# Kernel optimization log

Measured on AMD Instinct MI355X. Metric: run time of the kernel, lower is better.

The kernel has to match this reference:

```python
import jax, jax.numpy as jnp
import numpy as np

INPUT_SIZE = 128
HIDDEN_SIZE = 256
OUTPUT_SIZE = 64
BATCH = 128
SEQ_LEN = 2048


def _xavier(key, shape):
    fan_in, fan_out = shape[1], shape[0]
    std = (2.0 / (fan_in + fan_out)) ** 0.5
    return jax.random.normal(key, shape, dtype=jnp.float32) * std


def setup_inputs() -> dict:
    key = jax.random.key(0)
    ks = jax.random.split(key, 5)
    gru_in = INPUT_SIZE + OUTPUT_SIZE  # Jordan feedback: input concat prev output
    return {
        "x": jax.random.normal(ks[0], (BATCH, SEQ_LEN, INPUT_SIZE), dtype=jnp.float32),
        "w_ih": _xavier(ks[1], (3 * HIDDEN_SIZE, gru_in)),   # [r|z|n] input weights
        "w_hh": _xavier(ks[2], (3 * HIDDEN_SIZE, HIDDEN_SIZE)),
        "b_ih": jnp.zeros((3 * HIDDEN_SIZE,), dtype=jnp.float32),
        "b_hh": jnp.zeros((3 * HIDDEN_SIZE,), dtype=jnp.float32),
        "fc_w": _xavier(ks[3], (OUTPUT_SIZE, HIDDEN_SIZE)),
        "fc_b": jnp.zeros((OUTPUT_SIZE,), dtype=jnp.float32),
    }


def reference(x, w_ih, w_hh, b_ih, b_hh, fc_w, fc_b):
    B = x.shape[0]
    H = w_hh.shape[1]
    O = fc_w.shape[0]

    def step(carry, x_t):
        h, y_prev = carry  # h: [B,H], y_prev: [B,O]
        inp = jnp.concatenate([x_t, y_prev], axis=-1)       # [B, I+O]
        gi = inp @ w_ih.T + b_ih                            # [B, 3H]
        gh = h @ w_hh.T + b_hh                              # [B, 3H]
        i_r, i_z, i_n = jnp.split(gi, 3, axis=-1)
        h_r, h_z, h_n = jnp.split(gh, 3, axis=-1)
        r = jax.nn.sigmoid(i_r + h_r)
        z = jax.nn.sigmoid(i_z + h_z)
        n = jnp.tanh(i_n + r * h_n)
        h_new = (1.0 - z) * n + z * h                       # PyTorch GRU update
        y = jnp.tanh(h_new @ fc_w.T + fc_b)                 # Jordan output feedback
        return (h_new, y), None

    xs = jnp.swapaxes(x, 0, 1)  # [T, B, I] for scan over time
    h0 = jnp.zeros((B, H), dtype=x.dtype)
    y0 = jnp.zeros((B, O), dtype=x.dtype)
    (h_last, y_last), _ = jax.lax.scan(step, (h0, y0), xs)
    return y_last  # matches outputs[:, -1, :]
```

## Files before the change

### kernel.cpp

```cpp
#include <hip/hip_runtime.h>
#include <math.h>


#define TSTEPS 2048
#define ISZ 128

typedef _Float16 half8 __attribute__((ext_vector_type(8)));
typedef float f32x4 __attribute__((ext_vector_type(4)));
typedef unsigned int u32;
typedef unsigned int u32x4 __attribute__((ext_vector_type(4)));
typedef unsigned long long u64;

__device__ __forceinline__ f32x4 mfma16(half8 a, half8 b, f32x4 c) {
  return __builtin_amdgcn_mfma_f32_16x16x32_f16(a, b, c, 0, 0, 0);
}
__device__ __forceinline__ float sigm(float x) {
  return __builtin_amdgcn_rcpf(1.f + __expf(-x));
}
__device__ __forceinline__ float tanh_fast(float x) {
  return 1.f - 2.f * __builtin_amdgcn_rcpf(1.f + __expf(2.f * x));
}

__device__ __forceinline__ void st_pkt(void* p, u32x4 v) {
  asm volatile("global_store_dwordx4 %0, %1, off sc1" :: "v"(p), "v"(v) : "memory");
}
__device__ __forceinline__ void ld_pkt3_issue(const void* p1, const void* p2,
                                              const void* p3, u32x4& r1, u32x4& r2,
                                              u32x4& r3) {
  asm volatile("global_load_dwordx4 %0, %3, off sc1\n\t"
               "global_load_dwordx4 %1, %4, off sc1\n\t"
               "global_load_dwordx4 %2, %5, off sc1"
               : "=&v"(r1), "=&v"(r2), "=&v"(r3)
               : "v"(p1), "v"(p2), "v"(p3) : "memory");
}
__device__ __forceinline__ void ld_pkt3_wait(const void* p1, const void* p2,
                                             const void* p3, u32x4& r1, u32x4& r2,
                                             u32x4& r3) {
  asm volatile("global_load_dwordx4 %0, %3, off sc1\n\t"
               "global_load_dwordx4 %1, %4, off sc1\n\t"
               "global_load_dwordx4 %2, %5, off sc1\n\t"
               "s_waitcnt vmcnt(0)"
               : "=&v"(r1), "=&v"(r2), "=&v"(r3)
               : "v"(p1), "v"(p2), "v"(p3) : "memory");
}

__global__ __attribute__((amdgpu_flat_work_group_size(256, 256),
                          amdgpu_waves_per_eu(1, 1)))
void jordan_rnn(const float* __restrict__ xg, const float* __restrict__ w_ih,
                const float* __restrict__ w_hh, const float* __restrict__ b_ih,
                const float* __restrict__ b_hh, const float* __restrict__ fc_w,
                const float* __restrict__ fc_b, float* __restrict__ out,
                unsigned char* __restrict__ ws)
{
  const int tid  = threadIdx.x;
  const int lane = tid & 63;
  const int wv   = tid >> 6;
  const int n    = lane & 15;
  const int quad = lane >> 4;
  const int col  = blockIdx.x & 7;
  const int q    = blockIdx.x >> 3;
  const int u0   = q * 64 + wv * 16;
  const int b0   = col * 16;

  unsigned char* pay = ws;

  __shared__ _Float16 act[16][456];
  {
    unsigned int* za = (unsigned int*)&act[0][0];
    for (int i = tid; i < 3648; i += 256) za[i] = 0u;
  }

  half8 wr[14], wz[14], win[6], whn[8], wfc[8];
  {
    const int kq = quad * 8;
    const int ur = u0 + n, uz = 256 + u0 + n, un = 512 + u0 + n;
#pragma unroll
    for (int kk = 0; kk < 6; ++kk) {
      const float* pr = w_ih + ur * 192 + kk * 32 + kq;
      const float* pz = w_ih + uz * 192 + kk * 32 + kq;
      const float* pn = w_ih + un * 192 + kk * 32 + kq;
#pragma unroll
      for (int j = 0; j < 8; ++j) {
        wr[kk][j] = (_Float16)pr[j]; wz[kk][j] = (_Float16)pz[j]; win[kk][j] = (_Float16)pn[j];
      }
    }
#pragma unroll
    for (int kk = 0; kk < 8; ++kk) {
      const float* pr = w_hh + ur * 256 + kk * 32 + kq;
      const float* pz = w_hh + uz * 256 + kk * 32 + kq;
      const float* pn = w_hh + un * 256 + kk * 32 + kq;
#pragma unroll
      for (int j = 0; j < 8; ++j) {
        wr[6 + kk][j] = (_Float16)pr[j]; wz[6 + kk][j] = (_Float16)pz[j]; whn[kk][j] = (_Float16)pn[j];
      }
    }
#pragma unroll
    for (int kk = 0; kk < 8; ++kk) {
      const float* pf = fc_w + (wv * 16 + n) * 256 + kk * 32 + kq;
#pragma unroll
      for (int j = 0; j < 8; ++j) wfc[kk][j] = (_Float16)pf[j];
    }
  }
  const float br   = b_ih[u0 + n] + b_hh[u0 + n];
  const float bz   = b_ih[256 + u0 + n] + b_hh[256 + u0 + n];
  const float bin_ = b_ih[512 + u0 + n];
  const float bhn  = b_hh[512 + u0 + n];
  const float fcb  = fc_b[wv * 16 + n];

  float hprev[4] = {0.f, 0.f, 0.f, 0.f};

  const int xr = tid >> 4, xc = tid & 15;
  const int prow = lane >> 2, pc4 = lane & 3;
  const int sblk = tid >> 6, srem = tid & 63;
  const int srow = srem >> 2, sc4 = srem & 3;
  const int ok0 = 6 + 2 * q;
  const int fk0 = 2 * q;
  const int q1 = (q + 1) & 3, q2 = (q + 2) & 3, q3 = (q + 3) & 3;

  unsigned char* cb0 = pay + (size_t)col * 16384;
  unsigned char* cb1 = cb0 + 131072;
  const int poff = (q * 4 + wv) * 1024 + lane * 16;
  const int off1 = (q1 * 4 + sblk) * 1024 + srem * 16;
  const int off2 = (q2 * 4 + sblk) * 1024 + srem * 16;
  const int off3 = (q3 * 4 + sblk) * 1024 + srem * 16;

  const float* xbase = xg + (size_t)(b0 + xr) * TSTEPS * ISZ + xc * 8;
  float4 xv0, xv1;

  {
    float4 a = *(const float4*)xbase, b = *(const float4*)(xbase + 4);
    union { _Float16 h[8]; uint4 u; } pk;
    pk.h[0]=(_Float16)a.x; pk.h[1]=(_Float16)a.y; pk.h[2]=(_Float16)a.z; pk.h[3]=(_Float16)a.w;
    pk.h[4]=(_Float16)b.x; pk.h[5]=(_Float16)b.y; pk.h[6]=(_Float16)b.z; pk.h[7]=(_Float16)b.w;
    *(uint4*)&act[xr][xc * 8] = pk.u;
    xv0 = *(const float4*)(xbase + ISZ);
    xv1 = *(const float4*)(xbase + ISZ + 4);
  }
  __syncthreads();

  for (int t = 1; t <= TSTEPS; ++t) {
    const u32 tgt = (u32)(t - 1);
    unsigned char* cb = ((t - 1) & 1) ? cb1 : cb0;

    u32x4 r1, r2, r3;
    ld_pkt3_issue(cb + off1, cb + off2, cb + off3, r1, r2, r3);

    {
      u64 v = *(const u64*)&act[prow][192 + u0 + pc4 * 4];
      u32x4 pkt;
      pkt[0] = (u32)v; pkt[1] = (u32)(v >> 32); pkt[2] = tgt; pkt[3] = 0u;
      st_pkt(cb + poff, pkt);
    }

    f32x4 aR = {0,0,0,0}, aZ = {0,0,0,0}, aIN = {0,0,0,0}, aHN = {0,0,0,0};
    f32x4 accy = {0,0,0,0};
#pragma unroll
    for (int kk = 0; kk < 4; ++kk) {
      half8 af = *(const half8*)&act[n][kk * 32 + quad * 8];
      aR = mfma16(af, wr[kk], aR);
      aZ = mfma16(af, wz[kk], aZ);
      aIN = mfma16(af, win[kk], aIN);
    }
#pragma unroll
    for (int kk = 0; kk < 2; ++kk) {
      half8 af = *(const half8*)&act[n][(ok0 + kk) * 32 + quad * 8];
      aR = mfma16(af, wr[ok0 + kk], aR);
      aZ = mfma16(af, wz[ok0 + kk], aZ);
      aHN = mfma16(af, whn[ok0 - 6 + kk], aHN);
    }
#pragma unroll
    for (int kk = 0; kk < 2; ++kk) {
      half8 af = *(const half8*)&act[n][192 + (fk0 + kk) * 32 + quad * 8];
      accy = mfma16(af, wfc[fk0 + kk], accy);
    }

    __builtin_amdgcn_sched_barrier(0);
    asm volatile("s_waitcnt vmcnt(1)" : "+v"(r1), "+v"(r2), "+v"(r3) :: "memory");
    __builtin_amdgcn_sched_barrier(0);
    {
      int ok = (r1[2] >= tgt) && (r2[2] >= tgt) && (r3[2] >= tgt);
      while (!__all(ok)) {
        ld_pkt3_wait(cb + off1, cb + off2, cb + off3, r1, r2, r3);
        ok = (r1[2] >= tgt) && (r2[2] >= tgt) && (r3[2] >= tgt);
      }
    }
    *(u64*)&act[srow][192 + q1 * 64 + sblk * 16 + sc4 * 4] = ((u64)r1[1] << 32) | r1[0];
    *(u64*)&act[srow][192 + q2 * 64 + sblk * 16 + sc4 * 4] = ((u64)r2[1] << 32) | r2[0];
    *(u64*)&act[srow][192 + q3 * 64 + sblk * 16 + sc4 * 4] = ((u64)r3[1] << 32) | r3[0];
    __syncthreads();

#pragma unroll
    for (int kk = 6; kk < 14; ++kk) {
      if (kk == ok0 || kk == ok0 + 1) continue;
      half8 af = *(const half8*)&act[n][kk * 32 + quad * 8];
      aR = mfma16(af, wr[kk], aR);
      aZ = mfma16(af, wz[kk], aZ);
      aHN = mfma16(af, whn[kk - 6], aHN);
    }
#pragma unroll
    for (int kk = 0; kk < 8; ++kk) {
      if (kk == fk0 || kk == fk0 + 1) continue;
      half8 af = *(const half8*)&act[n][192 + kk * 32 + quad * 8];
      accy = mfma16(af, wfc[kk], accy);
    }
    if (t > 1) {
#pragma unroll
      for (int r = 0; r < 4; ++r)
        act[quad * 4 + r][128 + wv * 16 + n] = (_Float16)tanh_fast(accy[r] + fcb);
    }
    {
      union { _Float16 h[8]; uint4 u; } pk;
      pk.h[0]=(_Float16)xv0.x; pk.h[1]=(_Float16)xv0.y; pk.h[2]=(_Float16)xv0.z; pk.h[3]=(_Float16)xv0.w;
      pk.h[4]=(_Float16)xv1.x; pk.h[5]=(_Float16)xv1.y; pk.h[6]=(_Float16)xv1.z; pk.h[7]=(_Float16)xv1.w;
      *(uint4*)&act[xr][xc * 8] = pk.u;
      const size_t ts = (t + 1 < TSTEPS) ? (size_t)(t + 1) : (size_t)(TSTEPS - 1);
      xv0 = *(const float4*)(xbase + ts * ISZ);
      xv1 = *(const float4*)(xbase + ts * ISZ + 4);
    }
    __syncthreads();

#pragma unroll
    for (int kk = 4; kk < 6; ++kk) {
      half8 af = *(const half8*)&act[n][kk * 32 + quad * 8];
      aR = mfma16(af, wr[kk], aR);
      aZ = mfma16(af, wz[kk], aZ);
      aIN = mfma16(af, win[kk], aIN);
    }
#pragma unroll
    for (int r = 0; r < 4; ++r) {
      float rg = sigm(aR[r] + br);
      float zg = sigm(aZ[r] + bz);
      float nn = tanh_fast(aIN[r] + bin_ + rg * (aHN[r] + bhn));
      float hv = (1.f - zg) * nn + zg * hprev[r];
      hprev[r] = hv;
      act[quad * 4 + r][192 + u0 + n] = (_Float16)hv;
    }
    __syncthreads();
  }

  {
    const u32 tgt = (u32)TSTEPS;
    unsigned char* cb = (TSTEPS & 1) ? cb1 : cb0;

    u32x4 r1, r2, r3;
    ld_pkt3_issue(cb + off1, cb + off2, cb + off3, r1, r2, r3);
    {
      u64 v = *(const u64*)&act[prow][192 + u0 + pc4 * 4];
      u32x4 pkt;
      pkt[0] = (u32)v; pkt[1] = (u32)(v >> 32); pkt[2] = tgt; pkt[3] = 0u;
      st_pkt(cb + poff, pkt);
    }

    f32x4 accy = {0,0,0,0};
#pragma unroll
    for (int kk = 0; kk < 2; ++kk) {
      half8 af = *(const half8*)&act[n][192 + (fk0 + kk) * 32 + quad * 8];
      accy = mfma16(af, wfc[fk0 + kk], accy);
    }

    __builtin_amdgcn_sched_barrier(0);
    asm volatile("s_waitcnt vmcnt(1)" : "+v"(r1), "+v"(r2), "+v"(r3) :: "memory");
    __builtin_amdgcn_sched_barrier(0);
    {
      int ok = (r1[2] >= tgt) && (r2[2] >= tgt) && (r3[2] >= tgt);
      while (!__all(ok)) {
        ld_pkt3_wait(cb + off1, cb + off2, cb + off3, r1, r2, r3);
        ok = (r1[2] >= tgt) && (r2[2] >= tgt) && (r3[2] >= tgt);
      }
    }
    *(u64*)&act[srow][192 + q1 * 64 + sblk * 16 + sc4 * 4] = ((u64)r1[1] << 32) | r1[0];
    *(u64*)&act[srow][192 + q2 * 64 + sblk * 16 + sc4 * 4] = ((u64)r2[1] << 32) | r2[0];
    *(u64*)&act[srow][192 + q3 * 64 + sblk * 16 + sc4 * 4] = ((u64)r3[1] << 32) | r3[0];
    __syncthreads();

#pragma unroll
    for (int kk = 0; kk < 8; ++kk) {
      if (kk == fk0 || kk == fk0 + 1) continue;
      half8 af = *(const half8*)&act[n][192 + kk * 32 + quad * 8];
      accy = mfma16(af, wfc[kk], accy);
    }
    if (q == 0) {
#pragma unroll
      for (int r = 0; r < 4; ++r)
        out[(size_t)(b0 + quad * 4 + r) * 64 + wv * 16 + n] = tanh_fast(accy[r] + fcb);
    }
  }
}

extern "C" void kernel_launch(void* const* d_in, const int* in_sizes, int n_in,
                              void* d_out, int out_size, void* d_ws, size_t ws_size,
                              hipStream_t stream) {
  hipMemsetAsync(d_ws, 0, 262144, stream);
  jordan_rnn<<<dim3(32), dim3(256), 0, stream>>>(
      (const float*)d_in[0], (const float*)d_in[1], (const float*)d_in[2],
      (const float*)d_in[3], (const float*)d_in[4], (const float*)d_in[5],
      (const float*)d_in[6], (float*)d_out, (unsigned char*)d_ws);
}
```

Baseline: 4.573 ms.

## Publish hidden-state packets right after gate compute with checksum validation

Each block now sends its new hidden slice to peer blocks straight from registers at the end of the step, in MFMA column layout, rather than re-reading it from LDS at the start of the next step. This puts the send earlier on the cross-block critical path. An XOR checksum field guards against torn 16-byte packets, the poll loop gains an s_sleep, and only the q==0 blocks run the final exchange. In exchange, receivers now do scalar half-word LDS stores, wait for all loads instead of all but one, and may pick up extra latency from the sleep.

```diff
diff --git a/kernel.cpp b/kernel.cpp
--- a/kernel.cpp
+++ b/kernel.cpp
@@ -43,6 +43,7 @@
                : "=&v"(r1), "=&v"(r2), "=&v"(r3)
                : "v"(p1), "v"(p2), "v"(p3) : "memory");
 }
+#define PKT_OK(r, tgt) (((r)[2] >= (tgt)) && (((r)[0] ^ (r)[1] ^ (r)[2]) == (r)[3]))
 
 __global__ __attribute__((amdgpu_flat_work_group_size(256, 256),
                           amdgpu_waves_per_eu(1, 1)))
@@ -110,9 +111,9 @@
   float hprev[4] = {0.f, 0.f, 0.f, 0.f};
 
   const int xr = tid >> 4, xc = tid & 15;
-  const int prow = lane >> 2, pc4 = lane & 3;
   const int sblk = tid >> 6, srem = tid & 63;
-  const int srow = srem >> 2, sc4 = srem & 3;
+  const int cr = (srem >> 4) * 4;
+  const int cc = srem & 15;
   const int ok0 = 6 + 2 * q;
   const int fk0 = 2 * q;
   const int q1 = (q + 1) & 3, q2 = (q + 2) & 3, q3 = (q + 3) & 3;
@@ -145,13 +146,6 @@
     u32x4 r1, r2, r3;
     ld_pkt3_issue(cb + off1, cb + off2, cb + off3, r1, r2, r3);
 
-    {
-      u64 v = *(const u64*)&act[prow][192 + u0 + pc4 * 4];
-      u32x4 pkt;
-      pkt[0] = (u32)v; pkt[1] = (u32)(v >> 32); pkt[2] = tgt; pkt[3] = 0u;
-      st_pkt(cb + poff, pkt);
-    }
-
     f32x4 aR = {0,0,0,0}, aZ = {0,0,0,0}, aIN = {0,0,0,0}, aHN = {0,0,0,0};
     f32x4 accy = {0,0,0,0};
 #pragma unroll
@@ -175,18 +169,28 @@
     }
 
     __builtin_amdgcn_sched_barrier(0);
-    asm volatile("s_waitcnt vmcnt(1)" : "+v"(r1), "+v"(r2), "+v"(r3) :: "memory");
+    asm volatile("s_waitcnt vmcnt(0)" : "+v"(r1), "+v"(r2), "+v"(r3) :: "memory");
     __builtin_amdgcn_sched_barrier(0);
     {
-      int ok = (r1[2] >= tgt) && (r2[2] >= tgt) && (r3[2] >= tgt);
+      int ok = PKT_OK(r1, tgt) && PKT_OK(r2, tgt) && PKT_OK(r3, tgt);
       while (!__all(ok)) {
+        __builtin_amdgcn_s_sleep(1);
         ld_pkt3_wait(cb + off1, cb + off2, cb + off3, r1, r2, r3);
-        ok = (r1[2] >= tgt) && (r2[2] >= tgt) && (r3[2] >= tgt);
-      }
-    }
-    *(u64*)&act[srow][192 + q1 * 64 + sblk * 16 + sc4 * 4] = ((u64)r1[1] << 32) | r1[0];
-    *(u64*)&act[srow][192 + q2 * 64 + sblk * 16 + sc4 * 4] = ((u64)r2[1] << 32) | r2[0];
-    *(u64*)&act[srow][192 + q3 * 64 + sblk * 16 + sc4 * 4] = ((u64)r3[1] << 32) | r3[0];
+        ok = PKT_OK(r1, tgt) && PKT_OK(r2, tgt) && PKT_OK(r3, tgt);
+      }
+    }
+    {
+      union { u64 u; _Float16 h[4]; } w1, w2, w3;
+      w1.u = ((u64)r1[1] << 32) | r1[0];
+      w2.u = ((u64)r2[1] << 32) | r2[0];
+      w3.u = ((u64)r3[1] << 32) | r3[0];
+#pragma unroll
+      for (int r = 0; r < 4; ++r) {
+        act[cr + r][192 + q1 * 64 + sblk * 16 + cc] = w1.h[r];
+        act[cr + r][192 + q2 * 64 + sblk * 16 + cc] = w2.h[r];
+        act[cr + r][192 + q3 * 64 + sblk * 16 + cc] = w3.h[r];
+      }
+    }
     __syncthreads();
 
 #pragma unroll
@@ -226,30 +230,35 @@
       aZ = mfma16(af, wz[kk], aZ);
       aIN = mfma16(af, win[kk], aIN);
     }
-#pragma unroll
-    for (int r = 0; r < 4; ++r) {
-      float rg = sigm(aR[r] + br);
-      float zg = sigm(aZ[r] + bz);
-      float nn = tanh_fast(aIN[r] + bin_ + rg * (aHN[r] + bhn));
-      float hv = (1.f - zg) * nn + zg * hprev[r];
-      hprev[r] = hv;
-      act[quad * 4 + r][192 + u0 + n] = (_Float16)hv;
+    {
+      union { _Float16 h[4]; u64 u; } ph;
+#pragma unroll
+      for (int r = 0; r < 4; ++r) {
+        float rg = sigm(aR[r] + br);
+        float zg = sigm(aZ[r] + bz);
+        float nn = tanh_fast(aIN[r] + bin_ + rg * (aHN[r] + bhn));
+        float hv = (1.f - zg) * nn + zg * hprev[r];
+        hprev[r] = hv;
+        ph.h[r] = (_Float16)hv;
+      }
+      unsigned char* cbw = (t & 1) ? cb1 : cb0;
+      u32x4 pkt;
+      pkt[0] = (u32)ph.u; pkt[1] = (u32)(ph.u >> 32); pkt[2] = (u32)t;
+      pkt[3] = pkt[0] ^ pkt[1] ^ pkt[2];
+      st_pkt(cbw + poff, pkt);
+#pragma unroll
+      for (int r = 0; r < 4; ++r)
+        act[quad * 4 + r][192 + u0 + n] = ph.h[r];
     }
     __syncthreads();
   }
 
-  {
+  if (q == 0) {
     const u32 tgt = (u32)TSTEPS;
     unsigned char* cb = (TSTEPS & 1) ? cb1 : cb0;
 
     u32x4 r1, r2, r3;
     ld_pkt3_issue(cb + off1, cb + off2, cb + off3, r1, r2, r3);
-    {
-      u64 v = *(const u64*)&act[prow][192 + u0 + pc4 * 4];
-      u32x4 pkt;
-      pkt[0] = (u32)v; pkt[1] = (u32)(v >> 32); pkt[2] = tgt; pkt[3] = 0u;
-      st_pkt(cb + poff, pkt);
-    }
 
     f32x4 accy = {0,0,0,0};
 #pragma unroll
@@ -259,18 +268,28 @@
     }
 
     __builtin_amdgcn_sched_barrier(0);
-    asm volatile("s_waitcnt vmcnt(1)" : "+v"(r1), "+v"(r2), "+v"(r3) :: "memory");
+    asm volatile("s_waitcnt vmcnt(0)" : "+v"(r1), "+v"(r2), "+v"(r3) :: "memory");
     __builtin_amdgcn_sched_barrier(0);
     {
-      int ok = (r1[2] >= tgt) && (r2[2] >= tgt) && (r3[2] >= tgt);
+      int ok = PKT_OK(r1, tgt) && PKT_OK(r2, tgt) && PKT_OK(r3, tgt);
       while (!__all(ok)) {
+        __builtin_amdgcn_s_sleep(1);
         ld_pkt3_wait(cb + off1, cb + off2, cb + off3, r1, r2, r3);
-        ok = (r1[2] >= tgt) && (r2[2] >= tgt) && (r3[2] >= tgt);
-      }
-    }
-    *(u64*)&act[srow][192 + q1 * 64 + sblk * 16 + sc4 * 4] = ((u64)r1[1] << 32) | r1[0];
-    *(u64*)&act[srow][192 + q2 * 64 + sblk * 16 + sc4 * 4] = ((u64)r2[1] << 32) | r2[0];
-    *(u64*)&act[srow][192 + q3 * 64 + sblk * 16 + sc4 * 4] = ((u64)r3[1] << 32) | r3[0];
+        ok = PKT_OK(r1, tgt) && PKT_OK(r2, tgt) && PKT_OK(r3, tgt);
+      }
+    }
+    {
+      union { u64 u; _Float16 h[4]; } w1, w2, w3;
+      w1.u = ((u64)r1[1] << 32) | r1[0];
+      w2.u = ((u64)r2[1] << 32) | r2[0];
+      w3.u = ((u64)r3[1] << 32) | r3[0];
+#pragma unroll
+      for (int r = 0; r < 4; ++r) {
+        act[cr + r][192 + q1 * 64 + sblk * 16 + cc] = w1.h[r];
+        act[cr + r][192 + q2 * 64 + sblk * 16 + cc] = w2.h[r];
+        act[cr + r][192 + q3 * 64 + sblk * 16 + cc] = w3.h[r];
+      }
+    }
     __syncthreads();
 
 #pragma unroll
@@ -279,11 +298,9 @@
       half8 af = *(const half8*)&act[n][192 + kk * 32 + quad * 8];
       accy = mfma16(af, wfc[kk], accy);
     }
-    if (q == 0) {
-#pragma unroll
-      for (int r = 0; r < 4; ++r)
-        out[(size_t)(b0 + quad * 4 + r) * 64 + wv * 16 + n] = tanh_fast(accy[r] + fcb);
-    }
+#pragma unroll
+    for (int r = 0; r < 4; ++r)
+      out[(size_t)(b0 + quad * 4 + r) * 64 + wv * 16 + n] = tanh_fast(accy[r] + fcb);
   }
 }
 
```

Result: no change. 4.512 ms (-1.3%).
